# Kernel tuning notes

Measured on AMD Instinct MI355X. Metric: run time of the kernel, lower is better.

Reference implementation:

```python
import jax, jax.numpy as jnp
import numpy as np

IN_DIM, OUT_DIM, ATTN_DIM, N_REL = 128, 128, 64, 200
N_NODE, N_EDGE, N_QUERY = 50000, 500000, 64
VOCAB = 2 * N_REL + 1  # 401


def setup_inputs() -> dict:
    key = jax.random.key(0)
    ks = jax.random.split(key, 16)
    # edge table [E,7]: col0=r_idx, col2=rel, col4=sub, col5=obj, col6=time; cols 1,3 unused
    e = np.zeros((N_EDGE, 7), dtype=np.int64)
    e[:, 0] = np.asarray(jax.random.randint(ks[0], (N_EDGE,), 0, N_QUERY))
    e[:, 2] = np.asarray(jax.random.randint(ks[1], (N_EDGE,), 0, VOCAB))
    e[:, 4] = np.asarray(jax.random.randint(ks[2], (N_EDGE,), 0, N_NODE))
    e[:, 5] = np.asarray(jax.random.randint(ks[3], (N_EDGE,), 0, N_NODE))
    e[:, 6] = np.asarray(jax.random.randint(ks[4], (N_EDGE,), 0, 1000))
    s = 0.05
    return {
        "q_sub": jax.random.randint(ks[5], (N_QUERY,), 0, N_NODE),
        "q_rel": jax.random.randint(ks[6], (N_QUERY,), 0, VOCAB),
        "hidden": jax.random.normal(ks[7], (N_NODE, IN_DIM), jnp.float32),
        "edges": jnp.asarray(e),
        "n_node": N_NODE,
        "rela_embed": jax.random.normal(ks[8], (VOCAB, IN_DIM), jnp.float32),
        "Ws_W": jax.random.normal(ks[9], (ATTN_DIM, IN_DIM), jnp.float32) * s,
        "Wr_W": jax.random.normal(ks[10], (ATTN_DIM, IN_DIM), jnp.float32) * s,
        "Wqr_W": jax.random.normal(ks[11], (ATTN_DIM, IN_DIM), jnp.float32) * s,
        "Wqr_b": jnp.zeros((ATTN_DIM,), jnp.float32),
        "walpha_W": jax.random.normal(ks[12], (1, ATTN_DIM), jnp.float32) * s,
        "gateW_W": jax.random.normal(ks[13], (2 * IN_DIM, 3 * IN_DIM), jnp.float32) * s,
        "gateW_b": jnp.zeros((2 * IN_DIM,), jnp.float32),
        "ht_W": jax.random.normal(ks[14], (IN_DIM, 2 * IN_DIM), jnp.float32) * s,
        "ht_b": jnp.zeros((IN_DIM,), jnp.float32),
        "Wh_W": jax.random.normal(ks[15], (OUT_DIM, IN_DIM), jnp.float32) * s,
    }


def reference(q_sub, q_rel, hidden, edges, n_node, rela_embed,
              Ws_W, Wr_W, Wqr_W, Wqr_b, walpha_W,
              gateW_W, gateW_b, ht_W, ht_b, Wh_W):
    sub, rel, obj, r_idx = edges[:, 4], edges[:, 2], edges[:, 5], edges[:, 0]
    # unique+inverse on (rel,time) then embedding of rel == direct embedding lookup
    hr = rela_embed[rel]              # [E, in]
    hs = hidden[sub]                  # [E, in]
    h_qr = rela_embed[q_rel][r_idx]   # [E, in]
    # GateUnit(message=hr, factor=h_qr, hidden_state=hs)
    factors = jnp.concatenate([hr, h_qr, hs], axis=1)
    gates = jax.nn.sigmoid(factors @ gateW_W.T + gateW_b)
    update, reset = jnp.split(gates, 2, axis=1)
    cand = jnp.tanh(jnp.concatenate([hr, reset * hs], axis=1) @ ht_W.T + ht_b)
    message = (1.0 - update) * hs + update * cand
    # attention score
    pre = hs @ Ws_W.T + hr @ Wr_W.T + (h_qr @ Wqr_W.T + Wqr_b)
    alpha = jax.nn.leaky_relu(pre, 0.01) @ walpha_W.T  # [E,1]
    up_message = jax.nn.sigmoid(alpha) * message
    # scatter-sum over destination nodes + sqrt-degree normalization
    agg = jax.ops.segment_sum(up_message, obj, num_segments=n_node)
    deg = jax.ops.segment_sum(jnp.ones((up_message.shape[0], 1), jnp.float32), obj, num_segments=n_node)
    agg = agg / jnp.sqrt(deg + 0.0001)
    return agg @ Wh_W.T  # act = identity
```

## Files before the change

### kernel.cpp

```cpp
#include <hip/hip_runtime.h>

typedef unsigned short ushort_t;
typedef __attribute__((ext_vector_type(8))) short short8;
typedef __attribute__((ext_vector_type(4))) float f32x4;

#define DEV __device__ __forceinline__

DEV float sigm(float x) { return 1.0f / (1.0f + __expf(-x)); }
DEV float tanh_fast(float x) { return 1.0f - 2.0f / (__expf(2.0f * x) + 1.0f); }
DEV ushort_t f2bf(float v) {
    unsigned u = __float_as_uint(v);
    unsigned r = (u + 0x7fffu + ((u >> 16) & 1u)) >> 16;
    return (ushort_t)r;
}
DEV float bf2f(ushort_t h) { return __uint_as_float(((unsigned)h) << 16); }
DEV unsigned cvt_pk(float lo, float hi) {
    unsigned r;
    asm("v_cvt_pk_bf16_f32 %0, %1, %2" : "=v"(r) : "v"(lo), "v"(hi));
    return r;
}
DEV float dot4(float4 a, float4 b) {
    return fmaf(a.x, b.x, fmaf(a.y, b.y, fmaf(a.z, b.z, a.w * b.w)));
}

__global__ __launch_bounds__(256) void prep_kernel(
    const float* __restrict__ hidden, const float* __restrict__ gateW,
    const float* __restrict__ WsW,
    ushort_t* __restrict__ gate_hs, ushort_t* __restrict__ ws_hs,
    ushort_t* __restrict__ hsb, int nNode,
    const float* __restrict__ rela, const int* __restrict__ q_rel,
    const float* __restrict__ gateW_b,
    const float* __restrict__ WrW, const float* __restrict__ WqrW,
    const float* __restrict__ Wqr_b, const float* __restrict__ htW,
    const float* __restrict__ ht_b,
    float* __restrict__ grhr, float* __restrict__ gq,
    float* __restrict__ whr, float* __restrict__ wq,
    float* __restrict__ thr, int vocab,
    const int* __restrict__ edges, int nEdge, int* __restrict__ cnt,
    int nodeB, int tableB)
{
    __shared__ char smem[8192];
    int bid = blockIdx.x, t = threadIdx.x;

    if (bid < nodeB) {
        char* a_lds = smem;
        int w = t >> 6, l = t & 63;
        int lm = l & 15, lh = l >> 4;
        int nbase = bid * 32;

        for (int idx = t; idx < 1024; idx += 256) {
            int row = idx >> 5, c4 = idx & 31;
            int node = nbase + row;
            float4 v = (node < nNode) ? ((const float4*)hidden)[(size_t)node * 32 + c4]
                                      : float4{0.f, 0.f, 0.f, 0.f};
            uint2 p;
            p.x = cvt_pk(v.x, v.y);
            p.y = cvt_pk(v.z, v.w);
            *(uint2*)(a_lds + ((row * 256 + c4 * 8) ^ ((row & 7) << 4))) = p;
            if (node < nNode) *(uint2*)(hsb + (size_t)node * 128 + c4 * 4) = p;
        }

        short8 bfr[5][4];
#pragma unroll
        for (int nt = 0; nt < 5; nt++)
#pragma unroll
            for (int kt = 0; kt < 4; kt++) {
                int row = w * 80 + nt * 16 + lm;
                const float* src = (row < 256)
                    ? gateW + (size_t)row * 384 + 256 + kt * 32 + lh * 8
                    : WsW + (size_t)(row - 256) * 128 + kt * 32 + lh * 8;
                float4 f0 = *(const float4*)src;
                float4 f1 = *(const float4*)(src + 4);
                union { unsigned u[4]; short8 s; } tmp;
                tmp.u[0] = cvt_pk(f0.x, f0.y); tmp.u[1] = cvt_pk(f0.z, f0.w);
                tmp.u[2] = cvt_pk(f1.x, f1.y); tmp.u[3] = cvt_pk(f1.z, f1.w);
                bfr[nt][kt] = tmp.s;
            }
        __syncthreads();

        short8 afr[2][4];
#pragma unroll
        for (int mt = 0; mt < 2; mt++)
#pragma unroll
            for (int kt = 0; kt < 4; kt++) {
                int row = mt * 16 + lm;
                afr[mt][kt] = *(const short8*)(a_lds +
                    ((row * 256 + kt * 64 + lh * 16) ^ ((row & 7) << 4)));
            }
        f32x4 acc[2][5];
#pragma unroll
        for (int mt = 0; mt < 2; mt++)
#pragma unroll
            for (int nt = 0; nt < 5; nt++) acc[mt][nt] = (f32x4){0.f, 0.f, 0.f, 0.f};
#pragma unroll
        for (int kt = 0; kt < 4; kt++)
#pragma unroll
            for (int mt = 0; mt < 2; mt++)
#pragma unroll
                for (int nt = 0; nt < 5; nt++)
                    acc[mt][nt] = __builtin_amdgcn_mfma_f32_16x16x32_bf16(
                        afr[mt][kt], bfr[nt][kt], acc[mt][nt], 0, 0, 0);

#pragma unroll
        for (int mt = 0; mt < 2; mt++)
#pragma unroll
            for (int nt = 0; nt < 5; nt++) {
                int wrow = w * 80 + nt * 16 + lm;
#pragma unroll
                for (int r = 0; r < 4; r++) {
                    int node = nbase + mt * 16 + lh * 4 + r;
                    if (node < nNode) {
                        ushort_t v = f2bf(acc[mt][nt][r]);
                        if (wrow < 256)
                            gate_hs[(size_t)node * 256 + 2 * (wrow & 127) + (wrow >> 7)] = v;
                        else
                            ws_hs[(size_t)node * 64 + wrow - 256] = v;
                    }
                }
            }
    } else if (bid < nodeB + tableB) {
        float* x = (float*)smem;
        int b = bid - nodeB;
        bool isRel = b < vocab;
        int src = isRel ? b : q_rel[b - vocab];
        if (t < 128) x[t] = rela[src * 128 + t];
        __syncthreads();
        const float4* x4 = (const float4*)x;
        {
            const float4* wrow = (const float4*)(gateW + t * 384 + (isRel ? 0 : 128));
            float acc = isRel ? 0.0f : gateW_b[t];
#pragma unroll 8
            for (int i = 0; i < 32; i++) acc += dot4(wrow[i], x4[i]);
            float* dst = isRel ? (grhr + b * 256) : (gq + (b - vocab) * 256);
            dst[2 * (t & 127) + (t >> 7)] = acc;
        }
        if (isRel) {
            if (t < 192) {
                bool isWr = t < 64;
                int i = isWr ? t : (t - 64);
                const float* wp = isWr ? (WrW + i * 128) : (htW + i * 256);
                const float4* wrow = (const float4*)wp;
                float acc = isWr ? 0.0f : ht_b[i];
#pragma unroll 8
                for (int q = 0; q < 32; q++) acc += dot4(wrow[q], x4[q]);
                if (isWr) whr[b * 64 + i] = acc;
                else      thr[b * 128 + i] = acc;
            }
        } else {
            if (t < 64) {
                const float4* wrow = (const float4*)(WqrW + t * 128);
                float acc = Wqr_b[t];
#pragma unroll 8
                for (int q = 0; q < 32; q++) acc += dot4(wrow[q], x4[q]);
                wq[(b - vocab) * 64 + t] = acc;
            }
        }
    } else {
        int i = (bid - nodeB - tableB) * 256 + t;
        if (i < nEdge) atomicAdd(cnt + edges[(size_t)i * 7 + 5], 1);
    }
}

__global__ __launch_bounds__(256) void scan1_kernel(
    const int* __restrict__ cnt, int n, int* __restrict__ partials)
{
    __shared__ int s[256];
    int t = threadIdx.x;
    int i = blockIdx.x * 256 + t;
    s[t] = (i < n) ? cnt[i] : 0;
    __syncthreads();
    for (int o = 128; o > 0; o >>= 1) {
        if (t < o) s[t] += s[t + o];
        __syncthreads();
    }
    if (t == 0) partials[blockIdx.x] = s[0];
}

__global__ __launch_bounds__(256) void scan2_kernel(
    const int* __restrict__ cnt, int n, const int* __restrict__ partials,
    int nBlk, int* __restrict__ cursor)
{
    __shared__ int ps[256];
    __shared__ int loc[256];
    int t = threadIdx.x, b = blockIdx.x;
    ps[t] = (t < nBlk) ? partials[t] : 0;
    __syncthreads();
    for (int o = 1; o < 256; o <<= 1) {
        int v = (t >= o) ? ps[t - o] : 0;
        __syncthreads();
        ps[t] += v;
        __syncthreads();
    }
    int offset = (b > 0) ? ps[b - 1] : 0;
    int i = b * 256 + t;
    int v = (i < n) ? cnt[i] : 0;
    loc[t] = v;
    __syncthreads();
    for (int o = 1; o < 256; o <<= 1) {
        int x = (t >= o) ? loc[t - o] : 0;
        __syncthreads();
        loc[t] += x;
        __syncthreads();
    }
    if (i < n) cursor[i] = offset + loc[t] - v;
}

__global__ __launch_bounds__(256) void build_kernel(
    const int* __restrict__ edges, int nEdge, int* __restrict__ cursor,
    int4* __restrict__ sorted)
{
    int i = blockIdx.x * 256 + threadIdx.x;
    if (i < nEdge) {
        const int* er = edges + (size_t)i * 7;
        int obj = er[5];
        int s = atomicAdd(cursor + obj, 1);
        sorted[s] = make_int4(er[0], er[2], er[4], obj);
    }
}

__global__ __launch_bounds__(256, 8) void edge_kernel(
    const int4* __restrict__ sorted, int nEdge,
    const float* __restrict__ grhr, const float* __restrict__ gq,
    const float* __restrict__ whr, const float* __restrict__ wq,
    const float* __restrict__ thr,
    const ushort_t* __restrict__ gate_hs, const ushort_t* __restrict__ ws_hs,
    const ushort_t* __restrict__ hsb,
    const float* __restrict__ walpha, const float* __restrict__ htW,
    float* __restrict__ agg)
{
    __shared__ ushort_t xb[32 * 128];
    __shared__ ushort_t ub[32 * 128];
    __shared__ float sgaL[32];
    __shared__ int4 eds4[32];

    int t = threadIdx.x, w = t >> 6, l = t & 63;
    int lm = l & 15, lh = l >> 4;
    int n0 = w * 32;

    int nb = gridDim.x;
    int xcd = blockIdx.x & 7, lid = blockIdx.x >> 3;
    int q = nb >> 3, rr = nb & 7;
    int sbid = ((xcd < rr) ? xcd * (q + 1) : rr * (q + 1) + (xcd - rr) * q) + lid;
    int ebase = sbid * 32;

    if (t < 32) {
        int gi = ebase + t;
        eds4[t] = (gi < nEdge) ? sorted[gi] : make_int4(0, 0, 0, -1);
    }

    short8 bfr[2][4];
#pragma unroll
    for (int nt = 0; nt < 2; nt++)
#pragma unroll
        for (int kt = 0; kt < 4; kt++) {
            const float* src = htW + (size_t)(n0 + nt * 16 + lm) * 256 + 128 + kt * 32 + lh * 8;
            float4 f0 = *(const float4*)src;
            float4 f1 = *(const float4*)(src + 4);
            union { unsigned u[4]; short8 s; } tmp;
            tmp.u[0] = cvt_pk(f0.x, f0.y); tmp.u[1] = cvt_pk(f0.z, f0.w);
            tmp.u[2] = cvt_pk(f1.x, f1.y); tmp.u[3] = cvt_pk(f1.z, f1.w);
            bfr[nt][kt] = tmp.s;
        }
    float wal = walpha[l];
    __syncthreads();

    float aa8[8];
#pragma unroll
    for (int i = 0; i < 8; i++) {
        int e = w * 8 + i;
        int4 er = eds4[e];
        int ridx = er.x, rel = er.y, sub = er.z;
        ushort4 gp = *(const ushort4*)(gate_hs + (size_t)sub * 256 + 4 * l);
        float4 ga = *(const float4*)(grhr + (size_t)rel * 256 + 4 * l);
        float4 gb = *(const float4*)(gq + (size_t)ridx * 256 + 4 * l);
        unsigned hp = *(const unsigned*)(hsb + (size_t)sub * 128 + 2 * l);
        float aw = bf2f(ws_hs[(size_t)sub * 64 + l]) + whr[rel * 64 + l] + wq[ridx * 64 + l];
        float h0 = bf2f((ushort_t)(hp & 0xffffu));
        float h1 = bf2f((ushort_t)(hp >> 16));
        float u0 = sigm(ga.x + gb.x + bf2f(gp.x));
        float r0 = sigm(ga.y + gb.y + bf2f(gp.y));
        float u1 = sigm(ga.z + gb.z + bf2f(gp.z));
        float r1 = sigm(ga.w + gb.w + bf2f(gp.w));
        *(unsigned*)((char*)xb + ((e * 256 + 4 * l) ^ ((e & 7) << 4))) = cvt_pk(r0 * h0, r1 * h1);
        *(unsigned*)((char*)ub + ((e * 256 + 4 * l) ^ ((e & 7) << 5))) = cvt_pk(u0, u1);
        aa8[i] = fmaxf(aw, 0.01f * aw) * wal;
    }

    f32x4 acc[2][2];
#pragma unroll
    for (int mt = 0; mt < 2; mt++)
#pragma unroll
        for (int nt = 0; nt < 2; nt++) {
            int d = n0 + nt * 16 + lm;
#pragma unroll
            for (int r = 0; r < 4; r++) {
                int rel = eds4[mt * 16 + lh * 4 + r].y;
                acc[mt][nt][r] = thr[rel * 128 + d];
            }
        }

#pragma unroll
    for (int o = 32; o > 0; o >>= 1) {
#pragma unroll
        for (int i = 0; i < 8; i++) aa8[i] += __shfl_xor(aa8[i], o, 64);
    }
#pragma unroll
    for (int i = 0; i < 8; i++) {
        float s = sigm(aa8[i]);
        if (l == i) sgaL[w * 8 + i] = s;
    }
    __syncthreads();

    short8 afr[2][4];
#pragma unroll
    for (int mt = 0; mt < 2; mt++)
#pragma unroll
        for (int kt = 0; kt < 4; kt++) {
            int e = mt * 16 + lm;
            afr[mt][kt] = *(const short8*)((const char*)xb +
                ((e * 256 + kt * 64 + lh * 16) ^ ((e & 7) << 4)));
        }
#pragma unroll
    for (int kt = 0; kt < 4; kt++)
#pragma unroll
        for (int mt = 0; mt < 2; mt++)
#pragma unroll
            for (int nt = 0; nt < 2; nt++)
                acc[mt][nt] = __builtin_amdgcn_mfma_f32_16x16x32_bf16(
                    afr[mt][kt], bfr[nt][kt], acc[mt][nt], 0, 0, 0);

#pragma unroll
    for (int mt = 0; mt < 2; mt++)
#pragma unroll
        for (int nt = 0; nt < 2; nt++) {
            int d = n0 + nt * 16 + lm;
            float vals[4];
            int objs[4];
#pragma unroll
            for (int r = 0; r < 4; r++) {
                int e = mt * 16 + lh * 4 + r;
                int4 er = eds4[e];
                objs[r] = er.w;
                float h = bf2f(hsb[(size_t)er.z * 128 + d]);
                float u = bf2f(ub[((unsigned)(e * 256 + 2 * d) ^ ((e & 7) << 5)) >> 1]);
                float cand = tanh_fast(acc[mt][nt][r]);
                vals[r] = sgaL[e] * fmaf(u, cand - h, h);
            }
            float sum = vals[0];
            int prev = objs[0];
#pragma unroll
            for (int r = 1; r < 4; r++) {
                if (objs[r] == prev) {
                    sum += vals[r];
                } else {
                    if (prev >= 0) atomicAdd(agg + (size_t)prev * 128 + d, sum);
                    sum = vals[r];
                    prev = objs[r];
                }
            }
            if (prev >= 0) atomicAdd(agg + (size_t)prev * 128 + d, sum);
        }
}

__global__ __launch_bounds__(256) void final_kernel(
    const float* __restrict__ WhW, const int* __restrict__ degi,
    float* __restrict__ agg, int nNode)
{
    __shared__ char y_lds[64 * 256];
    int t = threadIdx.x, w = t >> 6, l = t & 63;
    int lm = l & 15, lh = l >> 4;
    int nbase = blockIdx.x * 64;

    short8 bfr[2][4];
#pragma unroll
    for (int nt = 0; nt < 2; nt++)
#pragma unroll
        for (int kt = 0; kt < 4; kt++) {
            const float* src = WhW + (size_t)(w * 32 + nt * 16 + lm) * 128 + kt * 32 + lh * 8;
            float4 f0 = *(const float4*)src;
            float4 f1 = *(const float4*)(src + 4);
            union { unsigned u[4]; short8 s; } tmp;
            tmp.u[0] = cvt_pk(f0.x, f0.y); tmp.u[1] = cvt_pk(f0.z, f0.w);
            tmp.u[2] = cvt_pk(f1.x, f1.y); tmp.u[3] = cvt_pk(f1.z, f1.w);
            bfr[nt][kt] = tmp.s;
        }

    for (int idx = t; idx < 2048; idx += 256) {
        int row = idx >> 5, c4 = idx & 31;
        int node = nbase + row;
        uint2 p = {0u, 0u};
        if (node < nNode) {
            float4 v = ((const float4*)agg)[(size_t)node * 32 + c4];
            float r = 1.0f / sqrtf((float)degi[node] + 1e-4f);
            p.x = cvt_pk(v.x * r, v.y * r);
            p.y = cvt_pk(v.z * r, v.w * r);
        }
        *(uint2*)(y_lds + ((row * 256 + c4 * 8) ^ ((row & 7) << 4))) = p;
    }
    __syncthreads();

    short8 afr[4][4];
#pragma unroll
    for (int mt = 0; mt < 4; mt++)
#pragma unroll
        for (int kt = 0; kt < 4; kt++) {
            int row = mt * 16 + lm;
            afr[mt][kt] = *(const short8*)(y_lds +
                ((row * 256 + kt * 64 + lh * 16) ^ ((row & 7) << 4)));
        }
    f32x4 acc[4][2];
#pragma unroll
    for (int mt = 0; mt < 4; mt++)
#pragma unroll
        for (int nt = 0; nt < 2; nt++) acc[mt][nt] = (f32x4){0.f, 0.f, 0.f, 0.f};
#pragma unroll
    for (int kt = 0; kt < 4; kt++)
#pragma unroll
        for (int mt = 0; mt < 4; mt++)
#pragma unroll
            for (int nt = 0; nt < 2; nt++)
                acc[mt][nt] = __builtin_amdgcn_mfma_f32_16x16x32_bf16(
                    afr[mt][kt], bfr[nt][kt], acc[mt][nt], 0, 0, 0);

#pragma unroll
    for (int mt = 0; mt < 4; mt++)
#pragma unroll
        for (int nt = 0; nt < 2; nt++) {
            int col = w * 32 + nt * 16 + lm;
#pragma unroll
            for (int r = 0; r < 4; r++) {
                int node = nbase + mt * 16 + lh * 4 + r;
                if (node < nNode) agg[(size_t)node * 128 + col] = acc[mt][nt][r];
            }
        }
}

extern "C" void kernel_launch(void* const* d_in, const int* in_sizes, int n_in,
                              void* d_out, int out_size, void* d_ws, size_t ws_size,
                              hipStream_t stream)
{
    const int*   q_rel   = (const int*)d_in[1];
    const float* hidden  = (const float*)d_in[2];
    const int*   edges   = (const int*)d_in[3];
    const float* rela    = (const float*)d_in[5];
    const float* WsW     = (const float*)d_in[6];
    const float* WrW     = (const float*)d_in[7];
    const float* WqrW    = (const float*)d_in[8];
    const float* Wqr_b   = (const float*)d_in[9];
    const float* walpha  = (const float*)d_in[10];
    const float* gateW   = (const float*)d_in[11];
    const float* gateW_b = (const float*)d_in[12];
    const float* htW     = (const float*)d_in[13];
    const float* ht_b    = (const float*)d_in[14];
    const float* WhW     = (const float*)d_in[15];

    int nNode  = in_sizes[2] / 128;
    int nEdge  = in_sizes[3] / 7;
    int vocab  = in_sizes[5] / 128;
    int nQuery = in_sizes[1];

    char* ws = (char*)d_ws;
    size_t off = 0;
    auto alloc = [&](size_t bytes) { size_t o = off; off += (bytes + 255) & ~(size_t)255; return o; };
    int*      cntO    = (int*)(ws + alloc((size_t)(nNode + 256) * 4));
    int*      cursorO = (int*)(ws + alloc((size_t)(nNode + 256) * 4));
    int*      partials= (int*)(ws + alloc(256 * 4));
    int4*     sorted  = (int4*)(ws + alloc((size_t)nEdge * 16));
    float*    grhr    = (float*)(ws + alloc((size_t)vocab * 256 * 4));
    float*    whr     = (float*)(ws + alloc((size_t)vocab * 64 * 4));
    float*    thr     = (float*)(ws + alloc((size_t)vocab * 128 * 4));
    float*    gq      = (float*)(ws + alloc((size_t)nQuery * 256 * 4));
    float*    wq      = (float*)(ws + alloc((size_t)nQuery * 64 * 4));
    ushort_t* gate_hs = (ushort_t*)(ws + alloc((size_t)nNode * 256 * 2));
    ushort_t* ws_hs   = (ushort_t*)(ws + alloc((size_t)nNode * 64 * 2));
    ushort_t* hsb     = (ushort_t*)(ws + alloc((size_t)nNode * 128 * 2));
    if (off > ws_size) return;

    float* agg = (float*)d_out;
    hipMemsetAsync(agg, 0, (size_t)nNode * 128 * 4, stream);
    hipMemsetAsync(cntO, 0, (size_t)(nNode + 256) * 4, stream);

    int nodeB  = (nNode + 31) / 32;
    int tableB = vocab + nQuery;
    int histB  = (nEdge + 255) / 256;
    prep_kernel<<<nodeB + tableB + histB, 256, 0, stream>>>(
        hidden, gateW, WsW, gate_hs, ws_hs, hsb, nNode,
        rela, q_rel, gateW_b, WrW, WqrW, Wqr_b, htW, ht_b,
        grhr, gq, whr, wq, thr, vocab,
        edges, nEdge, cntO, nodeB, tableB);

    int nScan = nNode + 1;
    int nBlk = (nScan + 255) / 256;
    scan1_kernel<<<nBlk, 256, 0, stream>>>(cntO, nScan, partials);
    scan2_kernel<<<nBlk, 256, 0, stream>>>(cntO, nScan, partials, nBlk, cursorO);
    build_kernel<<<(nEdge + 255) / 256, 256, 0, stream>>>(edges, nEdge, cursorO, sorted);

    int eblocks = (nEdge + 31) / 32;
    edge_kernel<<<eblocks, 256, 0, stream>>>(
        sorted, nEdge, grhr, gq, whr, wq, thr,
        gate_hs, ws_hs, hsb, walpha, htW, agg);

    int fblocks = (nNode + 63) / 64;
    final_kernel<<<fblocks, 256, 0, stream>>>(WhW, cntO, agg, nNode);
}
```

Before: 444.4 us.

## Make edge kernel persistent over edge batches with packed edge records

Each edge-kernel block now walks K=4 consecutive 32-edge batches and double-buffers the edge records in shared memory, so the per-block load and bf16 conversion of the ht_W fragments is paid once per four batches. Sorted edge records shrink from 16 to 8 bytes by bit-packing sub, r_idx and rel into one word. The epilogue also precomputes (1-u)*h and u in shared memory, removing the second gather of hs from global memory. In exchange there are fewer blocks with less parallelism, occupancy is lowered to 6 waves, and the packing assumes node ids fit in 16 bits and query ids in 6 bits.

```diff
diff --git a/kernel.cpp b/kernel.cpp
--- a/kernel.cpp
+++ b/kernel.cpp
@@ -207,19 +207,22 @@
 
 __global__ __launch_bounds__(256) void build_kernel(
     const int* __restrict__ edges, int nEdge, int* __restrict__ cursor,
-    int4* __restrict__ sorted)
+    uint2* __restrict__ sorted)
 {
     int i = blockIdx.x * 256 + threadIdx.x;
     if (i < nEdge) {
         const int* er = edges + (size_t)i * 7;
         int obj = er[5];
         int s = atomicAdd(cursor + obj, 1);
-        sorted[s] = make_int4(er[0], er[2], er[4], obj);
-    }
-}
-
-__global__ __launch_bounds__(256, 8) void edge_kernel(
-    const int4* __restrict__ sorted, int nEdge,
+        uint2 p;
+        p.x = (unsigned)er[4] | ((unsigned)er[0] << 16) | ((unsigned)er[2] << 22);
+        p.y = (unsigned)obj;
+        sorted[s] = p;
+    }
+}
+
+__global__ __launch_bounds__(256, 6) void edge_kernel(
+    const uint2* __restrict__ sorted, int nEdge, int nBatch, int K,
     const float* __restrict__ grhr, const float* __restrict__ gq,
     const float* __restrict__ whr, const float* __restrict__ wq,
     const float* __restrict__ thr,
@@ -229,9 +232,9 @@
     float* __restrict__ agg)
 {
     __shared__ ushort_t xb[32 * 128];
-    __shared__ ushort_t ub[32 * 128];
+    __shared__ unsigned ab[32 * 128];
     __shared__ float sgaL[32];
-    __shared__ int4 eds4[32];
+    __shared__ int4 eds4[2][32];
 
     int t = threadIdx.x, w = t >> 6, l = t & 63;
     int lm = l & 15, lh = l >> 4;
@@ -240,12 +243,20 @@
     int nb = gridDim.x;
     int xcd = blockIdx.x & 7, lid = blockIdx.x >> 3;
     int q = nb >> 3, rr = nb & 7;
-    int sbid = ((xcd < rr) ? xcd * (q + 1) : rr * (q + 1) + (xcd - rr) * q) + lid;
-    int ebase = sbid * 32;
+    int chunk = ((xcd < rr) ? xcd * (q + 1) : rr * (q + 1) + (xcd - rr) * q) + lid;
+    int b0 = chunk * K;
+    int b1 = min(b0 + K, nBatch);
+    if (b0 >= nBatch) return;
 
     if (t < 32) {
-        int gi = ebase + t;
-        eds4[t] = (gi < nEdge) ? sorted[gi] : make_int4(0, 0, 0, -1);
+        int gi = b0 * 32 + t;
+        if (gi < nEdge) {
+            uint2 p = sorted[gi];
+            eds4[0][t] = make_int4((int)((p.x >> 16) & 63u), (int)(p.x >> 22),
+                                   (int)(p.x & 0xffffu), (int)p.y);
+        } else {
+            eds4[0][t] = make_int4(0, 0, 0, -1);
+        }
     }
 
     short8 bfr[2][4];
@@ -264,102 +275,121 @@
     float wal = walpha[l];
     __syncthreads();
 
-    float aa8[8];
-#pragma unroll
-    for (int i = 0; i < 8; i++) {
-        int e = w * 8 + i;
-        int4 er = eds4[e];
-        int ridx = er.x, rel = er.y, sub = er.z;
-        ushort4 gp = *(const ushort4*)(gate_hs + (size_t)sub * 256 + 4 * l);
-        float4 ga = *(const float4*)(grhr + (size_t)rel * 256 + 4 * l);
-        float4 gb = *(const float4*)(gq + (size_t)ridx * 256 + 4 * l);
-        unsigned hp = *(const unsigned*)(hsb + (size_t)sub * 128 + 2 * l);
-        float aw = bf2f(ws_hs[(size_t)sub * 64 + l]) + whr[rel * 64 + l] + wq[ridx * 64 + l];
-        float h0 = bf2f((ushort_t)(hp & 0xffffu));
-        float h1 = bf2f((ushort_t)(hp >> 16));
-        float u0 = sigm(ga.x + gb.x + bf2f(gp.x));
-        float r0 = sigm(ga.y + gb.y + bf2f(gp.y));
-        float u1 = sigm(ga.z + gb.z + bf2f(gp.z));
-        float r1 = sigm(ga.w + gb.w + bf2f(gp.w));
-        *(unsigned*)((char*)xb + ((e * 256 + 4 * l) ^ ((e & 7) << 4))) = cvt_pk(r0 * h0, r1 * h1);
-        *(unsigned*)((char*)ub + ((e * 256 + 4 * l) ^ ((e & 7) << 5))) = cvt_pk(u0, u1);
-        aa8[i] = fmaxf(aw, 0.01f * aw) * wal;
-    }
-
-    f32x4 acc[2][2];
-#pragma unroll
-    for (int mt = 0; mt < 2; mt++)
-#pragma unroll
-        for (int nt = 0; nt < 2; nt++) {
-            int d = n0 + nt * 16 + lm;
-#pragma unroll
-            for (int r = 0; r < 4; r++) {
-                int rel = eds4[mt * 16 + lh * 4 + r].y;
-                acc[mt][nt][r] = thr[rel * 128 + d];
-            }
-        }
-
-#pragma unroll
-    for (int o = 32; o > 0; o >>= 1) {
-#pragma unroll
-        for (int i = 0; i < 8; i++) aa8[i] += __shfl_xor(aa8[i], o, 64);
-    }
-#pragma unroll
-    for (int i = 0; i < 8; i++) {
-        float s = sigm(aa8[i]);
-        if (l == i) sgaL[w * 8 + i] = s;
-    }
-    __syncthreads();
-
-    short8 afr[2][4];
-#pragma unroll
-    for (int mt = 0; mt < 2; mt++)
-#pragma unroll
-        for (int kt = 0; kt < 4; kt++) {
-            int e = mt * 16 + lm;
-            afr[mt][kt] = *(const short8*)((const char*)xb +
-                ((e * 256 + kt * 64 + lh * 16) ^ ((e & 7) << 4)));
-        }
-#pragma unroll
-    for (int kt = 0; kt < 4; kt++)
+    int cur = 0;
+    for (int b = b0; b < b1; ++b) {
+        float aa8[8];
+#pragma unroll
+        for (int i = 0; i < 8; i++) {
+            int e = w * 8 + i;
+            int4 er = eds4[cur][e];
+            int ridx = er.x, rel = er.y, sub = er.z;
+            ushort4 gp = *(const ushort4*)(gate_hs + (size_t)sub * 256 + 4 * l);
+            float4 ga = *(const float4*)(grhr + (size_t)rel * 256 + 4 * l);
+            float4 gb = *(const float4*)(gq + (size_t)ridx * 256 + 4 * l);
+            unsigned hp = *(const unsigned*)(hsb + (size_t)sub * 128 + 2 * l);
+            float aw = bf2f(ws_hs[(size_t)sub * 64 + l]) + whr[rel * 64 + l] + wq[ridx * 64 + l];
+            float h0 = bf2f((ushort_t)(hp & 0xffffu));
+            float h1 = bf2f((ushort_t)(hp >> 16));
+            float u0 = sigm(ga.x + gb.x + bf2f(gp.x));
+            float r0 = sigm(ga.y + gb.y + bf2f(gp.y));
+            float u1 = sigm(ga.z + gb.z + bf2f(gp.z));
+            float r1 = sigm(ga.w + gb.w + bf2f(gp.w));
+            *(unsigned*)((char*)xb + ((e * 256 + 4 * l) ^ ((e & 7) << 4))) = cvt_pk(r0 * h0, r1 * h1);
+            uint2 abp;
+            abp.x = cvt_pk((1.0f - u0) * h0, u0);
+            abp.y = cvt_pk((1.0f - u1) * h1, u1);
+            *(uint2*)((char*)ab + ((e * 512 + 8 * l) ^ (((e >> 2) & 3) << 6))) = abp;
+            aa8[i] = fmaxf(aw, 0.01f * aw) * wal;
+        }
+
+        f32x4 acc[2][2];
 #pragma unroll
         for (int mt = 0; mt < 2; mt++)
 #pragma unroll
-            for (int nt = 0; nt < 2; nt++)
-                acc[mt][nt] = __builtin_amdgcn_mfma_f32_16x16x32_bf16(
-                    afr[mt][kt], bfr[nt][kt], acc[mt][nt], 0, 0, 0);
-
-#pragma unroll
-    for (int mt = 0; mt < 2; mt++)
-#pragma unroll
-        for (int nt = 0; nt < 2; nt++) {
-            int d = n0 + nt * 16 + lm;
-            float vals[4];
-            int objs[4];
-#pragma unroll
-            for (int r = 0; r < 4; r++) {
-                int e = mt * 16 + lh * 4 + r;
-                int4 er = eds4[e];
-                objs[r] = er.w;
-                float h = bf2f(hsb[(size_t)er.z * 128 + d]);
-                float u = bf2f(ub[((unsigned)(e * 256 + 2 * d) ^ ((e & 7) << 5)) >> 1]);
-                float cand = tanh_fast(acc[mt][nt][r]);
-                vals[r] = sgaL[e] * fmaf(u, cand - h, h);
-            }
-            float sum = vals[0];
-            int prev = objs[0];
-#pragma unroll
-            for (int r = 1; r < 4; r++) {
-                if (objs[r] == prev) {
-                    sum += vals[r];
-                } else {
-                    if (prev >= 0) atomicAdd(agg + (size_t)prev * 128 + d, sum);
-                    sum = vals[r];
-                    prev = objs[r];
+            for (int nt = 0; nt < 2; nt++) {
+                int d = n0 + nt * 16 + lm;
+#pragma unroll
+                for (int r = 0; r < 4; r++) {
+                    int rel = eds4[cur][mt * 16 + lh * 4 + r].y;
+                    acc[mt][nt][r] = thr[rel * 128 + d];
                 }
             }
-            if (prev >= 0) atomicAdd(agg + (size_t)prev * 128 + d, sum);
-        }
+
+#pragma unroll
+        for (int o = 32; o > 0; o >>= 1) {
+#pragma unroll
+            for (int i = 0; i < 8; i++) aa8[i] += __shfl_xor(aa8[i], o, 64);
+        }
+#pragma unroll
+        for (int i = 0; i < 8; i++) {
+            float s = sigm(aa8[i]);
+            if (l == i) sgaL[w * 8 + i] = s;
+        }
+
+        if (b + 1 < b1 && t < 32) {
+            int gi = (b + 1) * 32 + t;
+            if (gi < nEdge) {
+                uint2 p = sorted[gi];
+                eds4[cur ^ 1][t] = make_int4((int)((p.x >> 16) & 63u), (int)(p.x >> 22),
+                                             (int)(p.x & 0xffffu), (int)p.y);
+            } else {
+                eds4[cur ^ 1][t] = make_int4(0, 0, 0, -1);
+            }
+        }
+        __syncthreads();
+
+        short8 afr[2][4];
+#pragma unroll
+        for (int mt = 0; mt < 2; mt++)
+#pragma unroll
+            for (int kt = 0; kt < 4; kt++) {
+                int e = mt * 16 + lm;
+                afr[mt][kt] = *(const short8*)((const char*)xb +
+                    ((e * 256 + kt * 64 + lh * 16) ^ ((e & 7) << 4)));
+            }
+#pragma unroll
+        for (int kt = 0; kt < 4; kt++)
+#pragma unroll
+            for (int mt = 0; mt < 2; mt++)
+#pragma unroll
+                for (int nt = 0; nt < 2; nt++)
+                    acc[mt][nt] = __builtin_amdgcn_mfma_f32_16x16x32_bf16(
+                        afr[mt][kt], bfr[nt][kt], acc[mt][nt], 0, 0, 0);
+
+#pragma unroll
+        for (int mt = 0; mt < 2; mt++)
+#pragma unroll
+            for (int nt = 0; nt < 2; nt++) {
+                int d = n0 + nt * 16 + lm;
+                float vals[4];
+                int objs[4];
+#pragma unroll
+                for (int r = 0; r < 4; r++) {
+                    int e = mt * 16 + lh * 4 + r;
+                    objs[r] = eds4[cur][e].w;
+                    float cand = tanh_fast(acc[mt][nt][r]);
+                    unsigned abw = *(const unsigned*)((const char*)ab +
+                        ((e * 512 + 4 * d) ^ (((e >> 2) & 3) << 6)));
+                    vals[r] = sgaL[e] * (bf2f((ushort_t)(abw & 0xffffu)) +
+                                         bf2f((ushort_t)(abw >> 16)) * cand);
+                }
+                float sum = vals[0];
+                int prev = objs[0];
+#pragma unroll
+                for (int r = 1; r < 4; r++) {
+                    if (objs[r] == prev) {
+                        sum += vals[r];
+                    } else {
+                        if (prev >= 0) atomicAdd(agg + (size_t)prev * 128 + d, sum);
+                        sum = vals[r];
+                        prev = objs[r];
+                    }
+                }
+                if (prev >= 0) atomicAdd(agg + (size_t)prev * 128 + d, sum);
+            }
+        __syncthreads();
+        cur ^= 1;
+    }
 }
 
 __global__ __launch_bounds__(256) void final_kernel(
@@ -465,7 +495,7 @@
     int*      cntO    = (int*)(ws + alloc((size_t)(nNode + 256) * 4));
     int*      cursorO = (int*)(ws + alloc((size_t)(nNode + 256) * 4));
     int*      partials= (int*)(ws + alloc(256 * 4));
-    int4*     sorted  = (int4*)(ws + alloc((size_t)nEdge * 16));
+    uint2*    sorted  = (uint2*)(ws + alloc((size_t)nEdge * 8));
     float*    grhr    = (float*)(ws + alloc((size_t)vocab * 256 * 4));
     float*    whr     = (float*)(ws + alloc((size_t)vocab * 64 * 4));
     float*    thr     = (float*)(ws + alloc((size_t)vocab * 128 * 4));
@@ -495,9 +525,11 @@
     scan2_kernel<<<nBlk, 256, 0, stream>>>(cntO, nScan, partials, nBlk, cursorO);
     build_kernel<<<(nEdge + 255) / 256, 256, 0, stream>>>(edges, nEdge, cursorO, sorted);
 
-    int eblocks = (nEdge + 31) / 32;
-    edge_kernel<<<eblocks, 256, 0, stream>>>(
-        sorted, nEdge, grhr, gq, whr, wq, thr,
+    int nBatch = (nEdge + 31) / 32;
+    int K = 4;
+    int nChunks = (nBatch + K - 1) / K;
+    edge_kernel<<<nChunks, 256, 0, stream>>>(
+        sorted, nEdge, nBatch, K, grhr, gq, whr, wq, thr,
         gate_hs, ws_hs, hsb, walpha, htW, agg);
 
     int fblocks = (nNode + 63) / 64;
```

Result: slower. 531.7 us (+19.6%).
